# Kernel tuning notes

Hardware: AMD Instinct MI355X
Metric: run time of the kernel (lower is better)

Reference implementation:

```python
import jax, jax.numpy as jnp
import numpy as np

IMG_H, IMG_W = 256, 704  # full image shape (img_metas['img_shape'])
EPS = 1e-5
B, N_CAM, D_REF, C_CH = 1, 6, 1, 256
HF, WF = 32, 88
DD = 64
BEV_H = BEV_W = 128
Q = BEV_H * BEV_W


def inverse_sigmoid(x, eps=1e-5):
    x = jnp.clip(x, 0.0, 1.0)
    return jnp.log(jnp.clip(x, eps) / jnp.clip(1.0 - x, eps))


def grid_sample_2d(feat, grid):
    # feat [N,C,H,W], grid [N,Hg,Wg,2] (x,y in [-1,1]); bilinear, zeros padding, align_corners=False
    Nn, C, H, W = feat.shape
    x = (grid[..., 0] + 1.0) * 0.5 * W - 0.5
    y = (grid[..., 1] + 1.0) * 0.5 * H - 0.5
    x0 = jnp.floor(x)
    y0 = jnp.floor(y)
    wx = x - x0
    wy = y - y0
    x0 = x0.astype(jnp.int32)
    y0 = y0.astype(jnp.int32)

    def gather(ix, iy):
        valid = (ix >= 0) & (ix < W) & (iy >= 0) & (iy < H)
        ixc = jnp.clip(ix, 0, W - 1)
        iyc = jnp.clip(iy, 0, H - 1)
        v = jax.vmap(lambda f, jx, jy: f[:, jy, jx])(feat, ixc, iyc)  # [N,C,Hg,Wg]
        return v * valid[:, None].astype(feat.dtype)

    return (gather(x0, y0) * ((1 - wx) * (1 - wy))[:, None]
            + gather(x0 + 1, y0) * (wx * (1 - wy))[:, None]
            + gather(x0, y0 + 1) * ((1 - wx) * wy)[:, None]
            + gather(x0 + 1, y0 + 1) * (wx * wy)[:, None])


def grid_sample_3d(vol, grid):
    # vol [N,C,D,H,W], grid [N,Dg,Hg,Wg,3] (x,y,z); trilinear, zeros padding, align_corners=False
    Nn, C, D, H, W = vol.shape
    x = (grid[..., 0] + 1.0) * 0.5 * W - 0.5
    y = (grid[..., 1] + 1.0) * 0.5 * H - 0.5
    z = (grid[..., 2] + 1.0) * 0.5 * D - 0.5
    x0 = jnp.floor(x); y0 = jnp.floor(y); z0 = jnp.floor(z)
    wx = x - x0; wy = y - y0; wz = z - z0
    x0 = x0.astype(jnp.int32); y0 = y0.astype(jnp.int32); z0 = z0.astype(jnp.int32)

    def gather(ix, iy, iz):
        valid = (ix >= 0) & (ix < W) & (iy >= 0) & (iy < H) & (iz >= 0) & (iz < D)
        ixc = jnp.clip(ix, 0, W - 1)
        iyc = jnp.clip(iy, 0, H - 1)
        izc = jnp.clip(iz, 0, D - 1)
        v = jax.vmap(lambda f, jx, jy, jz: f[:, jz, jy, jx])(vol, ixc, iyc, izc)
        return v * valid[:, None].astype(vol.dtype)

    return (gather(x0, y0, z0) * ((1 - wx) * (1 - wy) * (1 - wz))[:, None]
            + gather(x0 + 1, y0, z0) * (wx * (1 - wy) * (1 - wz))[:, None]
            + gather(x0, y0 + 1, z0) * ((1 - wx) * wy * (1 - wz))[:, None]
            + gather(x0 + 1, y0 + 1, z0) * (wx * wy * (1 - wz))[:, None]
            + gather(x0, y0, z0 + 1) * ((1 - wx) * (1 - wy) * wz)[:, None]
            + gather(x0 + 1, y0, z0 + 1) * (wx * (1 - wy) * wz)[:, None]
            + gather(x0, y0 + 1, z0 + 1) * ((1 - wx) * wy * wz)[:, None]
            + gather(x0 + 1, y0 + 1, z0 + 1) * (wx * wy * wz)[:, None])


def setup_inputs() -> dict:
    key = jax.random.key(0)
    ks = jax.random.split(key, 12)
    feat = jax.random.normal(ks[0], (B * N_CAM, C_CH, HF, WF), jnp.float32)
    bev_queries = jax.random.normal(ks[1], (B, Q, C_CH), jnp.float32)
    bev_pos = jax.random.normal(ks[2], (B, Q, C_CH), jnp.float32)
    reference_points = jax.random.uniform(ks[3], (B, D_REF, Q, 3), jnp.float32)
    pc_range = jnp.array([-51.2, -51.2, -5.0, 51.2, 51.2, 3.0], jnp.float32)
    # semi-realistic lidar->image projection matrices: intrinsics * axis-swap * yaw per camera
    f, cx, cy = 500.0, IMG_W / 2.0, IMG_H / 2.0
    K = np.array([[f, 0, cx, 0], [0, f, cy, 0], [0, 0, 1, 0], [0, 0, 0, 1]], np.float32)
    A = np.array([[0, -1, 0, 0], [0, 0, -1, 0], [1, 0, 0, 0], [0, 0, 0, 1]], np.float32)
    mats = []
    for i in range(N_CAM):
        th = 2.0 * np.pi * i / N_CAM
        c, s = np.cos(th), np.sin(th)
        R = np.array([[c, s, 0, 0], [-s, c, 0, 0], [0, 0, 1, 0], [0, 0, 0, 1]], np.float32)
        mats.append(K @ A @ R)
    lidar_to_img = jnp.asarray(np.stack(mats))[None]  # [1,N,4,4]
    depth_prob = jax.random.uniform(ks[4], (B * N_CAM, DD, HF, WF), jnp.float32)
    sc = 0.02
    return {
        'feat': feat, 'bev_queries': bev_queries, 'bev_pos': bev_pos,
        'reference_points': reference_points, 'pc_range': pc_range,
        'lidar_to_img': lidar_to_img, 'depth_prob': depth_prob,
        'w_pos': jax.random.normal(ks[5], (C_CH, 1), jnp.float32) * sc,
        'b_pos': jnp.zeros((1,), jnp.float32),
        'w_img': jax.random.normal(ks[6], (C_CH, N_CAM * 2), jnp.float32) * sc,
        'b_img': jnp.zeros((N_CAM * 2,), jnp.float32),
        'w_att': jax.random.normal(ks[7], (C_CH, N_CAM), jnp.float32) * sc,
        'b_att': jnp.zeros((N_CAM,), jnp.float32),
        'conv_w': jax.random.normal(ks[8], (C_CH, C_CH, 3, 3), jnp.float32) * sc,
        'conv_b': jnp.zeros((C_CH,), jnp.float32),
        'bn_gamma': jnp.ones((C_CH,), jnp.float32),
        'bn_beta': jnp.zeros((C_CH,), jnp.float32),
        'bn_mean': jnp.zeros((C_CH,), jnp.float32),
        'bn_var': jnp.ones((C_CH,), jnp.float32),
        'se_w': jax.random.normal(ks[9], (C_CH, C_CH), jnp.float32) * sc,
        'se_b': jnp.zeros((C_CH,), jnp.float32),
        'cbam_w': jax.random.normal(ks[10], (1, 2, 7, 7), jnp.float32) * 0.05,
        'cbam_b': jnp.zeros((1,), jnp.float32),
        'bev_h': BEV_H, 'bev_w': BEV_W,
    }


def reference(feat, bev_queries, bev_pos, reference_points, pc_range, lidar_to_img, depth_prob,
              w_pos, b_pos, w_img, b_img, w_att, b_att, conv_w, conv_b,
              bn_gamma, bn_beta, bn_mean, bn_var, se_w, se_b, cbam_w, cbam_b, bev_h, bev_w):
    Bq, Qn = bev_queries.shape[:2]
    D = reference_points.shape[1]
    N = lidar_to_img.shape[1]
    BN, C, Hf, Wf = feat.shape
    q = bev_queries + bev_pos
    pos_offset = q @ w_pos + b_pos  # [B,Q,1] (only_use_height)
    z = jax.nn.sigmoid(inverse_sigmoid(reference_points[..., 2:3]) + pos_offset[:, None])
    rp = jnp.concatenate([reference_points[..., :2], z], axis=-1)  # [B,D,Q,3]
    attn = (q @ w_att + b_att).reshape(Bq, 1, Qn, N, 1)
    img_off = q @ w_img + b_img  # [B,Q,2N]
    # unnormalize to lidar coords; apply_3d_transformation == identity (no aug)
    pts = rp * (pc_range[3:] - pc_range[:3]) + pc_range[:3]
    pts4 = jnp.concatenate([pts, jnp.ones_like(pts[..., :1])], axis=-1)  # [B,D,Q,4]
    cam = jnp.einsum('bnij,bdqj->dbnqi', lidar_to_img, pts4)  # [D,B,N,Q,4]
    ref_depth = cam[..., 2:3]
    mask = ref_depth > EPS
    xy = cam[..., :2] / jnp.maximum(cam[..., 2:3], EPS)
    xy = xy / jnp.array([IMG_W, IMG_H], dtype=xy.dtype)
    xy = (xy - 0.5) * 2.0
    mask = mask & (xy[..., 0:1] > -1.0) & (xy[..., 0:1] < 1.0) & (xy[..., 1:2] > -1.0) & (xy[..., 1:2] < 1.0)
    Dd = depth_prob.shape[1]
    ref_depth = (ref_depth / Dd - 0.5) * 2.0
    mask = mask & (ref_depth > -1.0) & (ref_depth < 1.0)
    bev_mask = jnp.transpose(mask, (1, 4, 3, 2, 0)).astype(feat.dtype)  # [B,1,Q,N,D]
    off = img_off.reshape(Bq, Qn, N, 2).transpose(0, 2, 1, 3)[None] / jnp.array([Wf, Hf], dtype=feat.dtype)
    xy = xy + off  # [D,B,N,Q,2]
    grid = xy.transpose(1, 2, 3, 0, 4).reshape(BN, Qn, D, 2)
    sampled = grid_sample_2d(feat, grid).reshape(Bq, N, C, Qn, D).transpose(0, 2, 3, 1, 4)  # [B,C,Q,N,D]
    grid3 = jnp.concatenate([xy, ref_depth], axis=-1).transpose(1, 2, 3, 0, 4).reshape(BN, 1, Qn, D, 3)
    dp = grid_sample_3d(depth_prob[:, None], grid3).reshape(Bq, N, 1, Qn, D).transpose(0, 2, 3, 1, 4)
    bev_mask = jnp.nan_to_num(dp) * bev_mask
    w = jax.nn.sigmoid(attn) * jnp.nan_to_num(bev_mask)
    agg = (jnp.nan_to_num(sampled) * w)[..., 0].sum(-1)  # [B,C,Q] (D==1)
    x = agg.reshape(Bq, C, bev_h, bev_w)
    dn = ('NCHW', 'OIHW', 'NCHW')
    x = jax.lax.conv_general_dilated(x, conv_w, (1, 1), ((1, 1), (1, 1)), dimension_numbers=dn) + conv_b[None, :, None, None]
    x = (x - bn_mean[None, :, None, None]) * (bn_gamma / jnp.sqrt(bn_var + 1e-5))[None, :, None, None] + bn_beta[None, :, None, None]
    x = jax.nn.relu(x)
    s = x.mean(axis=(2, 3))  # SE: global avg pool + 1x1 conv + sigmoid
    x = x * jax.nn.sigmoid(s @ se_w.T + se_b)[:, :, None, None]
    a = jnp.concatenate([x.max(axis=1, keepdims=True), x.mean(axis=1, keepdims=True)], axis=1)  # CBAM spatial
    a = jax.lax.conv_general_dilated(a, cbam_w, (1, 1), ((3, 3), (3, 3)), dimension_numbers=dn) + cbam_b[None, :, None, None]
    x = x * jax.nn.sigmoid(a)
    out = x.reshape(Bq, C, bev_h * bev_w).transpose(0, 2, 1)
    return out, rp
```

## Files before the change

### kernel.cpp

```cpp
#include <hip/hip_runtime.h>
#include <math.h>

#define QN   16384
#define CCH  256
#define NCAM 6
#define HFD  32
#define WFD  88
#define DDD  64
#define BEVH 128
#define BEVW 128
#define IMGW 704.0f
#define IMGH 256.0f
#define EPSV 1e-5f

typedef __attribute__((ext_vector_type(8))) short bf8_t;
typedef __attribute__((ext_vector_type(8))) unsigned short us8;
typedef __attribute__((ext_vector_type(4))) unsigned short us4;
typedef __attribute__((ext_vector_type(4))) float f4_t;

__device__ __forceinline__ float sigmoidf_(float x){ return 1.0f/(1.0f+__expf(-x)); }

__device__ __forceinline__ unsigned short f2bf(float f){
    unsigned int b = __float_as_uint(f);
    b += 0x7FFFu + ((b >> 16) & 1u);
    return (unsigned short)(b >> 16);
}
__device__ __forceinline__ float bf2f(unsigned short u){
    return __uint_as_float(((unsigned int)u) << 16);
}

__global__ __launch_bounds__(256) void k_prep(const float* __restrict__ feat, unsigned short* __restrict__ feat_tH,
                                              const float* __restrict__ cw, unsigned short* __restrict__ wtH,
                                              const float* __restrict__ se_w, float* __restrict__ se_wT,
                                              float* __restrict__ ssum){
    int b = blockIdx.x;
    if (b < 4224){
        __shared__ float tile[32][33];
        int n   = b / 704;
        int rem = b - n*704;
        int cb  = (rem / 88) * 32;
        int pb  = (rem % 88) * 32;
        int tx = threadIdx.x & 31, ty = threadIdx.x >> 5;
        for (int r = ty; r < 32; r += 8)
            tile[r][tx] = feat[(size_t)(n*256 + cb + r)*2816 + pb + tx];
        __syncthreads();
        for (int r = ty; r < 32; r += 8)
            feat_tH[(size_t)(n*2816 + pb + r)*256 + cb + tx] = f2bf(tile[tx][r]);
    } else if (b < 6528){
        int b2 = b - 4224;
        if (b2 == 0) ssum[threadIdx.x] = 0.f;
        int idx = b2*256 + threadIdx.x;
        int ci = idx & 255;
        int co = (idx >> 8) & 255;
        int kk = idx >> 16;
        int kh = kk/3, kw = kk - kh*3;
        int chunk = ci >> 6, ciin = ci & 63;
        size_t dst = ((((size_t)(kh*4 + chunk)*3 + kw)*256 + co) << 6) + ciin;
        wtH[dst] = f2bf(cw[(size_t)(co*256 + ci)*9 + kk]);
    } else {
        __shared__ float tile[32][33];
        int tb = b - 6528;
        int rb_ = (tb >> 3) * 32;
        int cb_ = (tb & 7) * 32;
        int tx = threadIdx.x & 31, ty = threadIdx.x >> 5;
        for (int r = ty; r < 32; r += 8)
            tile[r][tx] = se_w[(size_t)(rb_ + r)*256 + cb_ + tx];
        __syncthreads();
        for (int r = ty; r < 32; r += 8)
            se_wT[(size_t)(cb_ + r)*256 + rb_ + tx] = tile[tx][r];
    }
}

__global__ __launch_bounds__(256) void k_proj(
    const float* __restrict__ bq, const float* __restrict__ bpos,
    const float* __restrict__ refp,
    const float* __restrict__ w_pos, const float* __restrict__ b_pos,
    const float* __restrict__ w_img, const float* __restrict__ w_att,
    float* __restrict__ Sg, float* __restrict__ out_rp)
{
    __shared__ float wlf[19][260];
    __shared__ unsigned short Aq[64][264];
    __shared__ float sl[64][20];
    int tid = threadIdx.x;
    int lane = tid & 63, wid = tid >> 6;
    int l15 = lane & 15, quad = lane >> 4;
    int q0 = blockIdx.x * 64;

    wlf[0][tid] = w_pos[tid];
    #pragma unroll
    for (int r = 0; r < 6; r++){
        int idx = r*256 + tid;
        int c = idx / 6, j = idx - 6*c;
        wlf[1 + j][c] = w_att[idx];
    }
    #pragma unroll
    for (int r = 0; r < 12; r++){
        int idx = r*256 + tid;
        int c = idx / 12, j = idx - 12*c;
        wlf[7 + j][c] = w_img[idx];
    }
    #pragma unroll
    for (int r = 0; r < 16; r++){
        int row = r*4 + wid;
        int cc  = lane * 4;
        float4 a = *(const float4*)(bq   + (size_t)(q0+row)*CCH + cc);
        float4 b = *(const float4*)(bpos + (size_t)(q0+row)*CCH + cc);
        us4 o;
        o.x = f2bf(a.x+b.x); o.y = f2bf(a.y+b.y); o.z = f2bf(a.z+b.z); o.w = f2bf(a.w+b.w);
        *(us4*)&Aq[row][cc] = o;
    }
    __syncthreads();

    f4_t acc0 = (f4_t){0.f,0.f,0.f,0.f};
    f4_t acc1 = (f4_t){0.f,0.f,0.f,0.f};
    #pragma unroll
    for (int kc = 0; kc < 8; kc++){
        bf8_t af = *(bf8_t*)&Aq[wid*16 + l15][kc*32 + quad*8];
        bf8_t b0, b1;
        {
            const float* wr = &wlf[l15][kc*32 + quad*8];
            float4 w0 = *(const float4*)wr;
            float4 w1 = *(const float4*)(wr + 4);
            b0[0]=(short)f2bf(w0.x); b0[1]=(short)f2bf(w0.y); b0[2]=(short)f2bf(w0.z); b0[3]=(short)f2bf(w0.w);
            b0[4]=(short)f2bf(w1.x); b0[5]=(short)f2bf(w1.y); b0[6]=(short)f2bf(w1.z); b0[7]=(short)f2bf(w1.w);
        }
        if (l15 < 3){
            const float* wr = &wlf[16 + l15][kc*32 + quad*8];
            float4 w0 = *(const float4*)wr;
            float4 w1 = *(const float4*)(wr + 4);
            b1[0]=(short)f2bf(w0.x); b1[1]=(short)f2bf(w0.y); b1[2]=(short)f2bf(w0.z); b1[3]=(short)f2bf(w0.w);
            b1[4]=(short)f2bf(w1.x); b1[5]=(short)f2bf(w1.y); b1[6]=(short)f2bf(w1.z); b1[7]=(short)f2bf(w1.w);
        } else {
            b1 = (bf8_t){0,0,0,0,0,0,0,0};
        }
        acc0 = __builtin_amdgcn_mfma_f32_16x16x32_bf16(af, b0, acc0, 0, 0, 0);
        acc1 = __builtin_amdgcn_mfma_f32_16x16x32_bf16(af, b1, acc1, 0, 0, 0);
    }
    #pragma unroll
    for (int r = 0; r < 4; r++){
        int qq = wid*16 + quad*4 + r;
        sl[qq][l15] = acc0[r];
        if (l15 < 3) sl[qq][16 + l15] = acc1[r];
    }
    __syncthreads();

    if (tid < 64){
        int q = q0 + tid;
        float pos_off = sl[tid][0] + b_pos[0];
        float rx = refp[q*3+0], ry = refp[q*3+1], rz = refp[q*3+2];
        float zc_ = fminf(fmaxf(rz, 0.f), 1.f);
        float inv = logf(fmaxf(zc_, EPSV) / fmaxf(1.f - zc_, EPSV));
        float znew = sigmoidf_(inv + pos_off);
        out_rp[q*3+0] = rx; out_rp[q*3+1] = ry; out_rp[q*3+2] = znew;
        sl[tid][19] = znew;
    }
    __syncthreads();

    for (int i = tid; i < 64*20; i += 256)
        Sg[(size_t)q0*20 + i] = ((const float*)sl)[i];
}

__global__ __launch_bounds__(256) void k_geomagg(
    const float* __restrict__ refp, const float* __restrict__ pcr,
    const float* __restrict__ l2i, const float* __restrict__ dpr,
    const float* __restrict__ b_img, const float* __restrict__ b_att,
    const float* __restrict__ Sg, const unsigned short* __restrict__ feat_tH,
    unsigned short* __restrict__ aggH)
{
    __shared__ float sgl[8][20];
    __shared__ int   so_l[192];
    __shared__ float sw_l[192];
    int q0 = blockIdx.x * 8;
    int tid = threadIdx.x;
    int wid = tid >> 6, lane = tid & 63;

    if (tid < 160) ((float*)sgl)[tid] = Sg[(size_t)q0*20 + tid];
    __syncthreads();

    {
        int sub = lane >> 5;
        int n   = lane & 31;
        if (n < NCAM){
            int ql = wid*2 + sub;
            int q  = q0 + ql;
            float att  = sgl[ql][1+n] + b_att[n];
            float offx = (sgl[ql][7+2*n] + b_img[2*n])   / (float)WFD;
            float offy = (sgl[ql][8+2*n] + b_img[2*n+1]) / (float)HFD;
            float znew = sgl[ql][19];
            float rx = refp[q*3+0], ry = refp[q*3+1];
            float lo0=pcr[0], lo1=pcr[1], lo2=pcr[2];
            float hi0=pcr[3], hi1=pcr[4], hi2=pcr[5];
            float px = rx*(hi0-lo0)+lo0, py = ry*(hi1-lo1)+lo1, pz = znew*(hi2-lo2)+lo2;
            const float* M = l2i + n*16;
            float cx = M[0]*px + M[1]*py + M[2]*pz  + M[3];
            float cy = M[4]*px + M[5]*py + M[6]*pz  + M[7];
            float cz = M[8]*px + M[9]*py + M[10]*pz + M[11];
            bool m = cz > EPSV;
            float zdiv = fmaxf(cz, EPSV);
            float u = (cx/zdiv)/IMGW; u = (u - 0.5f)*2.f;
            float v = (cy/zdiv)/IMGH; v = (v - 0.5f)*2.f;
            m = m && (u > -1.f) && (u < 1.f) && (v > -1.f) && (v < 1.f);
            float rdn = (cz/(float)DDD - 0.5f)*2.f;
            m = m && (rdn > -1.f) && (rdn < 1.f);

            int base = ql*24 + n*4;
            float wq = 0.f, xs = 0.f, ys = 0.f;
            if (m){
                float u2 = u + offx, v2 = v + offy;
                xs = (u2 + 1.f)*0.5f*WFD - 0.5f;
                ys = (v2 + 1.f)*0.5f*HFD - 0.5f;
                float zs = (rdn + 1.f)*0.5f*DDD - 0.5f;
                float fx = floorf(xs), fy = floorf(ys), fz = floorf(zs);
                int x0=(int)fx, y0=(int)fy, z0=(int)fz;
                float wx = xs-fx, wy = ys-fy, wz = zs-fz;
                float dp = 0.f;
                const float* vol = dpr + (size_t)n*DDD*HFD*WFD;
                #pragma unroll
                for (int dz=0; dz<2; dz++)
                #pragma unroll
                for (int dy=0; dy<2; dy++)
                #pragma unroll
                for (int dx=0; dx<2; dx++){
                    int ix=x0+dx, iy=y0+dy, iz=z0+dz;
                    if (ix>=0 && ix<WFD && iy>=0 && iy<HFD && iz>=0 && iz<DDD){
                        float ww = (dx?wx:1.f-wx)*(dy?wy:1.f-wy)*(dz?wz:1.f-wz);
                        dp += ww * vol[(size_t)(iz*HFD+iy)*WFD + ix];
                    }
                }
                wq = sigmoidf_(att) * dp;
            }
            if (m && wq != 0.f){
                float fx = floorf(xs), fy = floorf(ys);
                int x0=(int)fx, y0=(int)fy;
                float wx = xs-fx, wy = ys-fy;
                float cwv[4] = {(1.f-wx)*(1.f-wy), wx*(1.f-wy), (1.f-wx)*wy, wx*wy};
                int xi[4] = {x0, x0+1, x0, x0+1};
                int yi[4] = {y0, y0, y0+1, y0+1};
                #pragma unroll
                for (int k=0;k<4;k++){
                    bool ok = (xi[k]>=0 && xi[k]<WFD && yi[k]>=0 && yi[k]<HFD);
                    so_l[base+k] = ok ? ((n*HFD + yi[k])*WFD + xi[k]) : 0;
                    sw_l[base+k] = ok ? wq*cwv[k] : 0.f;
                }
            } else {
                #pragma unroll
                for (int k=0;k<4;k++){ so_l[base+k] = 0; sw_l[base+k] = 0.f; }
            }
        }
    }
    __syncthreads();

    int cnt;
    {
        int half = lane >> 5, li = lane & 31;
        int ql = wid*2 + half;
        bool p = false;
        int   so_v = 0;
        float sw_v = 0.f;
        if (li < 24){
            sw_v = sw_l[ql*24 + li];
            so_v = so_l[ql*24 + li];
            p = (sw_v != 0.f);
        }
        unsigned long long m64 = __ballot(p);
        unsigned int hm = (unsigned int)(half ? (m64 >> 32) : m64);
        cnt = __popc(hm);
        int pos = __popc(hm & ((1u << li) - 1u));
        if (p){
            so_l[ql*24 + pos] = so_v;
            sw_l[ql*24 + pos] = sw_v;
        }
    }

    {
        int half = lane >> 5, li = lane & 31;
        int c8 = li * 8;
        int ql = wid*2 + half;
        float a[8] = {0.f,0.f,0.f,0.f,0.f,0.f,0.f,0.f};
        for (int k=0;k<cnt;k++){
            float w = sw_l[ql*24+k];
            us8 v = *(const us8*)(feat_tH + (size_t)so_l[ql*24+k]*CCH + c8);
            #pragma unroll
            for (int j=0;j<8;j++) a[j] += w * bf2f((unsigned short)v[j]);
        }
        us8 o;
        #pragma unroll
        for (int j=0;j<8;j++) o[j] = f2bf(a[j]);
        *(us8*)(aggH + (size_t)(q0+ql)*CCH + c8) = o;
    }
}

__global__ __launch_bounds__(256, 3) void k_conv2(const unsigned short* __restrict__ aggH,
    const unsigned short* __restrict__ wtH, const float* __restrict__ conv_b,
    const float* __restrict__ bn_g, const float* __restrict__ bn_b,
    const float* __restrict__ bn_m, const float* __restrict__ bn_v,
    float* __restrict__ xN, float* __restrict__ ssum)
{
    __shared__ unsigned short Al[130][72];
    __shared__ unsigned short Bl[3][64][72];
    __shared__ float sacc[64];

    int h   = blockIdx.x;
    int co0 = blockIdx.y * 64;
    int tid  = threadIdx.x;
    int lane = tid & 63, wid = tid >> 6;
    int m_q = (wid & 1) * 64;
    int n_q = (wid >> 1) * 32;
    int l15 = lane & 15, quad = lane >> 4;

    f4_t acc[4][2];
    #pragma unroll
    for (int i=0;i<4;i++)
    #pragma unroll
    for (int j=0;j<2;j++) acc[i][j] = (f4_t){0.f,0.f,0.f,0.f};

    int arow = tid >> 1;
    int aseg = (tid & 1) * 32;

    if (tid < 16){
        int r = (tid >> 3) ? 129 : 0;
        int sg = (tid & 7) * 8;
        *(us8*)&Al[r][sg] = (us8){0,0,0,0,0,0,0,0};
    }
    if (tid < 64) sacc[tid] = 0.f;

    us8 ra[4], rb[3][2];
    const us8 z8 = (us8){0,0,0,0,0,0,0,0};

    #define LOADSTAGE(s) { \
        int kh_ = (s) >> 2; \
        int ph_ = h + kh_ - 1; \
        if (ph_ >= 0 && ph_ < BEVH){ \
            const unsigned short* ap_ = aggH + ((size_t)(ph_*BEVW + arow)*CCH + (((s) & 3) << 6) + aseg); \
            ra[0] = *(const us8*)ap_;        ra[1] = *(const us8*)(ap_ + 8); \
            ra[2] = *(const us8*)(ap_ + 16); ra[3] = *(const us8*)(ap_ + 24); \
        } else { ra[0]=z8; ra[1]=z8; ra[2]=z8; ra[3]=z8; } \
        const unsigned short* bp_ = wtH + (size_t)(s)*49152 + (size_t)co0*64; \
        _Pragma("unroll") \
        for (int kw_=0; kw_<3; kw_++){ \
            _Pragma("unroll") \
            for (int j_=0; j_<2; j_++) \
                rb[kw_][j_] = *(const us8*)(bp_ + kw_*16384 + (j_*256 + tid)*8); \
        } \
    }

    LOADSTAGE(0);
    for (int s=0; s<12; s++){
        __syncthreads();
        *(us8*)&Al[arow+1][aseg]      = ra[0];
        *(us8*)&Al[arow+1][aseg+8]    = ra[1];
        *(us8*)&Al[arow+1][aseg+16]   = ra[2];
        *(us8*)&Al[arow+1][aseg+24]   = ra[3];
        {
            int bco = tid >> 3;
            int ciin = (tid & 7) * 8;
            #pragma unroll
            for (int kw_=0; kw_<3; kw_++){
                #pragma unroll
                for (int j_=0; j_<2; j_++)
                    *(us8*)&Bl[kw_][j_*32 + bco][ciin] = rb[kw_][j_];
            }
        }
        __syncthreads();
        if (s < 11) LOADSTAGE(s+1);
        #pragma unroll
        for (int ks=0; ks<2; ks++){
            #pragma unroll
            for (int kw=0; kw<3; kw++){
                bf8_t af[4], bfr[2];
                #pragma unroll
                for (int i=0;i<4;i++) af[i]  = *(bf8_t*)&Al[m_q + i*16 + l15 + kw][ks*32 + quad*8];
                #pragma unroll
                for (int j=0;j<2;j++) bfr[j] = *(bf8_t*)&Bl[kw][n_q + j*16 + l15][ks*32 + quad*8];
                #pragma unroll
                for (int i=0;i<4;i++)
                #pragma unroll
                for (int j=0;j<2;j++)
                    acc[i][j] = __builtin_amdgcn_mfma_f32_16x16x32_bf16(af[i], bfr[j], acc[i][j], 0, 0, 0);
            }
        }
    }
    #undef LOADSTAGE

    #pragma unroll
    for (int j=0;j<2;j++){
        int col = n_q + j*16 + l15;
        int co = co0 + col;
        float sc = bn_g[co] * rsqrtf(bn_v[co] + 1e-5f);
        float sh = bn_b[co] - bn_m[co]*sc;
        float cb = conv_b[co];
        float part = 0.f;
        #pragma unroll
        for (int i=0;i<4;i++){
            #pragma unroll
            for (int r=0;r<4;r++){
                int m = m_q + i*16 + quad*4 + r;
                int p = h*BEVW + m;
                float y = fmaxf((acc[i][j][r] + cb)*sc + sh, 0.f);
                xN[(size_t)p*CCH + co] = y;
                part += y;
            }
        }
        atomicAdd(&sacc[col], part);
    }
    __syncthreads();
    if (tid < 64) atomicAdd(&ssum[co0 + tid], sacc[tid]);
}

__global__ __launch_bounds__(256) void k_maps2(const float* __restrict__ xN,
    const float* __restrict__ ssum, const float* __restrict__ se_wT, const float* __restrict__ se_b,
    float* __restrict__ scale_g, float* __restrict__ amax, float* __restrict__ amean)
{
    __shared__ float smv[256];
    __shared__ float scl[256];
    int t = threadIdx.x;
    smv[t] = ssum[t] * (1.f/16384.f);
    __syncthreads();
    float a0=0.f, a1=0.f, a2=0.f, a3=0.f;
    for (int k=0; k<256; k+=4){
        a0 += smv[k]   * se_wT[(size_t)(k  )*256 + t];
        a1 += smv[k+1] * se_wT[(size_t)(k+1)*256 + t];
        a2 += smv[k+2] * se_wT[(size_t)(k+2)*256 + t];
        a3 += smv[k+3] * se_wT[(size_t)(k+3)*256 + t];
    }
    float sv = sigmoidf_(se_b[t] + ((a0+a1)+(a2+a3)));
    scl[t] = sv;
    if (blockIdx.x == 0) scale_g[t] = sv;
    __syncthreads();

    int wid = t >> 6, lane = t & 63;
    int p0 = blockIdx.x * 64;
    float4 sc = *(const float4*)&scl[lane*4];
    for (int i=0; i<16; i++){
        int p = p0 + i*4 + wid;
        float4 v = *(const float4*)&xN[(size_t)p*CCH + lane*4];
        float a = v.x*sc.x, b = v.y*sc.y, c = v.z*sc.z, d = v.w*sc.w;
        float mx = fmaxf(fmaxf(a,b), fmaxf(c,d));
        float sm = a+b+c+d;
        #pragma unroll
        for (int off=1; off<64; off<<=1){
            mx = fmaxf(mx, __shfl_xor(mx, off, 64));
            sm += __shfl_xor(sm, off, 64);
        }
        if (lane == 0){ amax[p] = mx; amean[p] = sm*(1.f/256.f); }
    }
}

__global__ __launch_bounds__(256) void k_final2(const float* __restrict__ xN,
    const float* __restrict__ scale_g, const float* __restrict__ amax, const float* __restrict__ amean,
    const float* __restrict__ cw, const float* __restrict__ cb, float* __restrict__ out)
{
    __shared__ float am2[7][128];
    __shared__ float av2[7][128];
    __shared__ float wcb[98];
    __shared__ float scl[256];
    __shared__ float amap_l[64];

    int b = blockIdx.x;
    int h  = b >> 1;
    int w0 = (b & 1) * 64;
    int t = threadIdx.x;

    scl[t] = scale_g[t];
    if (t < 98) wcb[t] = cw[t];
    for (int idx = t; idx < 896; idx += 256){
        int r = idx >> 7, c = idx & 127;
        int ph = h + r - 3;
        bool ok = (ph >= 0 && ph < BEVH);
        am2[r][c] = ok ? amax[ph*BEVW + c] : 0.f;
        av2[r][c] = ok ? amean[ph*BEVW + c] : 0.f;
    }
    __syncthreads();

    if (t < 64){
        int px = w0 + t;
        float acc = cb[0];
        #pragma unroll
        for (int kh=0; kh<7; kh++){
            #pragma unroll
            for (int kw=0; kw<7; kw++){
                int pw = px + kw - 3;
                if (pw >= 0 && pw < BEVW)
                    acc += am2[kh][pw]*wcb[kh*7+kw] + av2[kh][pw]*wcb[49 + kh*7+kw];
            }
        }
        amap_l[t] = sigmoidf_(acc);
    }
    __syncthreads();

    int lane = t & 63, sub = t >> 6;
    int c4 = lane * 4;
    float4 sc = *(const float4*)&scl[c4];
    for (int i=0; i<16; i++){
        int pxl = sub*16 + i;
        int p = h*BEVW + w0 + pxl;
        float am = amap_l[pxl];
        float4 v = *(const float4*)&xN[(size_t)p*CCH + c4];
        float4 o;
        o.x = v.x*sc.x*am; o.y = v.y*sc.y*am; o.z = v.z*sc.z*am; o.w = v.w*sc.w*am;
        *(float4*)&out[(size_t)p*CCH + c4] = o;
    }
}

extern "C" void kernel_launch(void* const* d_in, const int* in_sizes, int n_in,
                              void* d_out, int out_size, void* d_ws, size_t ws_size,
                              hipStream_t stream) {
    const float* feat   = (const float*)d_in[0];
    const float* bq     = (const float*)d_in[1];
    const float* bpos   = (const float*)d_in[2];
    const float* refp   = (const float*)d_in[3];
    const float* pcr    = (const float*)d_in[4];
    const float* l2i    = (const float*)d_in[5];
    const float* dpr    = (const float*)d_in[6];
    const float* w_pos  = (const float*)d_in[7];
    const float* b_pos  = (const float*)d_in[8];
    const float* w_img  = (const float*)d_in[9];
    const float* b_img  = (const float*)d_in[10];
    const float* w_att  = (const float*)d_in[11];
    const float* b_att  = (const float*)d_in[12];
    const float* conv_w = (const float*)d_in[13];
    const float* conv_b = (const float*)d_in[14];
    const float* bn_g   = (const float*)d_in[15];
    const float* bn_b   = (const float*)d_in[16];
    const float* bn_m   = (const float*)d_in[17];
    const float* bn_v   = (const float*)d_in[18];
    const float* se_w   = (const float*)d_in[19];
    const float* se_b   = (const float*)d_in[20];
    const float* cbw    = (const float*)d_in[21];
    const float* cbb    = (const float*)d_in[22];
    float* out = (float*)d_out;

    float* ws = (float*)d_ws;
    size_t o = 0;
    unsigned short* feat_tH = (unsigned short*)(ws + o); o += (size_t)6*2816*128;
    unsigned short* wtH  = (unsigned short*)(ws + o); o += (size_t)9*256*128;
    unsigned short* aggH = (unsigned short*)(ws + o); o += (size_t)QN*128;
    float* xN      = ws + o;  o += (size_t)QN*256;
    float* se_wT   = ws + o;  o += (size_t)256*256;
    float* Sg      = ws + o;  o += (size_t)QN*20;
    float* ssum    = ws + o;  o += 256;
    float* scale_g = ws + o;  o += 256;
    float* amax    = ws + o;  o += QN;
    float* amean   = ws + o;  o += QN;

    k_prep<<<6592, 256, 0, stream>>>(feat, feat_tH, conv_w, wtH, se_w, se_wT, ssum);
    k_proj<<<256, 256, 0, stream>>>(bq, bpos, refp, w_pos, b_pos, w_img, w_att,
                                    Sg, out + (size_t)QN*256);
    k_geomagg<<<2048, 256, 0, stream>>>(refp, pcr, l2i, dpr, b_img, b_att,
                                        Sg, feat_tH, aggH);
    k_conv2<<<dim3(128,4), 256, 0, stream>>>(aggH, wtH, conv_b, bn_g, bn_b, bn_m, bn_v, xN, ssum);
    k_maps2<<<256, 256, 0, stream>>>(xN, ssum, se_wT, se_b, scale_g, amax, amean);
    k_final2<<<256, 256, 0, stream>>>(xN, scale_g, amax, amean, cbw, cbb, out);
}
```

Measured before the change: 214.3 us.

## Stream conv weights directly into double-buffered swizzled LDS via global_load_lds

The conv kernel's weight tiles now go straight from global memory into LDS using the direct global-to-LDS load builtin, instead of staging through registers. The tile is double-buffered so the next stage's weights load while the current stage's MFMAs run, and the layout uses an XOR swizzle in place of padding to avoid bank conflicts. Occupancy hint drops from 3 to 2 blocks per SU because LDS use grows, and the A tile padding changes. This removes register pressure and VGPR-to-LDS store instructions, but there is a risk that async LDS writes are not properly waited on before the barrier, and occupancy is lower.

```diff
diff --git a/kernel.cpp b/kernel.cpp
--- a/kernel.cpp
+++ b/kernel.cpp
@@ -28,6 +28,10 @@
 __device__ __forceinline__ float bf2f(unsigned short u){
     return __uint_as_float(((unsigned int)u) << 16);
 }
+
+#define GLD16(gp_, lp_) __builtin_amdgcn_global_load_lds( \
+    (const __attribute__((address_space(1))) unsigned int*)(gp_), \
+    (__attribute__((address_space(3))) unsigned int*)(lp_), 16, 0, 0)
 
 __global__ __launch_bounds__(256) void k_prep(const float* __restrict__ feat, unsigned short* __restrict__ feat_tH,
                                               const float* __restrict__ cw, unsigned short* __restrict__ wtH,
@@ -290,14 +294,14 @@
     }
 }
 
-__global__ __launch_bounds__(256, 3) void k_conv2(const unsigned short* __restrict__ aggH,
+__global__ __launch_bounds__(256, 2) void k_conv2(const unsigned short* __restrict__ aggH,
     const unsigned short* __restrict__ wtH, const float* __restrict__ conv_b,
     const float* __restrict__ bn_g, const float* __restrict__ bn_b,
     const float* __restrict__ bn_m, const float* __restrict__ bn_v,
     float* __restrict__ xN, float* __restrict__ ssum)
 {
-    __shared__ unsigned short Al[130][72];
-    __shared__ unsigned short Bl[3][64][72];
+    __shared__ unsigned short Al[130][76];
+    __shared__ unsigned short BlL[2][3][64][64];
     __shared__ float sacc[64];
 
     int h   = blockIdx.x;
@@ -307,6 +311,7 @@
     int m_q = (wid & 1) * 64;
     int n_q = (wid >> 1) * 32;
     int l15 = lane & 15, quad = lane >> 4;
+    int swB = l15 & 7;
 
     f4_t acc[4][2];
     #pragma unroll
@@ -324,10 +329,10 @@
     }
     if (tid < 64) sacc[tid] = 0.f;
 
-    us8 ra[4], rb[3][2];
+    us8 ra[4];
     const us8 z8 = (us8){0,0,0,0,0,0,0,0};
 
-    #define LOADSTAGE(s) { \
+    #define LOADA(s) { \
         int kh_ = (s) >> 2; \
         int ph_ = h + kh_ - 1; \
         if (ph_ >= 0 && ph_ < BEVH){ \
@@ -335,34 +340,37 @@
             ra[0] = *(const us8*)ap_;        ra[1] = *(const us8*)(ap_ + 8); \
             ra[2] = *(const us8*)(ap_ + 16); ra[3] = *(const us8*)(ap_ + 24); \
         } else { ra[0]=z8; ra[1]=z8; ra[2]=z8; ra[3]=z8; } \
+    }
+
+    #define LOADB(s, bq_) { \
         const unsigned short* bp_ = wtH + (size_t)(s)*49152 + (size_t)co0*64; \
+        int srcsw_ = (((tid & 7) ^ ((tid >> 3) & 7)) << 3); \
         _Pragma("unroll") \
         for (int kw_=0; kw_<3; kw_++){ \
             _Pragma("unroll") \
-            for (int j_=0; j_<2; j_++) \
-                rb[kw_][j_] = *(const us8*)(bp_ + kw_*16384 + (j_*256 + tid)*8); \
+            for (int j_=0; j_<2; j_++){ \
+                const unsigned short* gp_ = bp_ + kw_*16384 + (size_t)(j_*32 + (tid>>3))*64 + srcsw_; \
+                unsigned short* lp_ = &BlL[bq_][kw_][j_*32 + wid*8][0]; \
+                GLD16(gp_, lp_); \
+            } \
         } \
     }
 
-    LOADSTAGE(0);
+    LOADA(0);
+    LOADB(0, 0);
+    int buf = 0;
+
     for (int s=0; s<12; s++){
         __syncthreads();
         *(us8*)&Al[arow+1][aseg]      = ra[0];
         *(us8*)&Al[arow+1][aseg+8]    = ra[1];
         *(us8*)&Al[arow+1][aseg+16]   = ra[2];
         *(us8*)&Al[arow+1][aseg+24]   = ra[3];
-        {
-            int bco = tid >> 3;
-            int ciin = (tid & 7) * 8;
-            #pragma unroll
-            for (int kw_=0; kw_<3; kw_++){
-                #pragma unroll
-                for (int j_=0; j_<2; j_++)
-                    *(us8*)&Bl[kw_][j_*32 + bco][ciin] = rb[kw_][j_];
-            }
-        }
         __syncthreads();
-        if (s < 11) LOADSTAGE(s+1);
+        if (s < 11){
+            LOADA(s+1);
+            LOADB(s+1, buf^1);
+        }
         #pragma unroll
         for (int ks=0; ks<2; ks++){
             #pragma unroll
@@ -371,7 +379,10 @@
                 #pragma unroll
                 for (int i=0;i<4;i++) af[i]  = *(bf8_t*)&Al[m_q + i*16 + l15 + kw][ks*32 + quad*8];
                 #pragma unroll
-                for (int j=0;j<2;j++) bfr[j] = *(bf8_t*)&Bl[kw][n_q + j*16 + l15][ks*32 + quad*8];
+                for (int j=0;j<2;j++){
+                    int slot = (((ks<<2) | quad) ^ swB);
+                    bfr[j] = *(bf8_t*)&BlL[buf][kw][n_q + j*16 + l15][slot*8];
+                }
                 #pragma unroll
                 for (int i=0;i<4;i++)
                 #pragma unroll
@@ -379,8 +390,10 @@
                     acc[i][j] = __builtin_amdgcn_mfma_f32_16x16x32_bf16(af[i], bfr[j], acc[i][j], 0, 0, 0);
             }
         }
-    }
-    #undef LOADSTAGE
+        buf ^= 1;
+    }
+    #undef LOADA
+    #undef LOADB
 
     #pragma unroll
     for (int j=0;j<2;j++){
```

New measurement: 210.8 us. No clear change (-1.6%).
